# Kernel optimization log

Measured on AMD Instinct MI355X. Metric: run time of the kernel, lower is better.

Reference implementation:

```python
import jax, jax.numpy as jnp
import numpy as np

D_MODEL, N_HEADS, D_HEAD = 1024, 16, 64
B, T = 4, 2048


def setup_inputs() -> dict:
    key = jax.random.key(0)
    k1, k2, k3 = jax.random.split(key, 3)
    x = jax.random.normal(k1, (B, T, D_MODEL), dtype=jnp.float32)
    w_qkv = jax.random.normal(k2, (3 * N_HEADS * D_HEAD, D_MODEL), dtype=jnp.float32) * 0.02
    w_out = jax.random.normal(k3, (D_MODEL, N_HEADS * D_HEAD), dtype=jnp.float32) * 0.02
    return {"x": x, "w_qkv": w_qkv, "w_out": w_out}


def reference(x, w_qkv, w_out):
    Bx, Tx, Dx = x.shape
    scale = D_HEAD ** (-0.5)
    qkv = jnp.einsum('btd,ed->bte', x, w_qkv)  # [B,T,3*H*Dh]
    q, k, v = jnp.split(qkv, 3, axis=-1)
    def heads(t):  # [B,T,H*Dh] -> [B,H,T,Dh]
        return t.reshape(Bx, Tx, N_HEADS, D_HEAD).transpose(0, 2, 1, 3)
    q, k, v = heads(q), heads(k), heads(v)
    att = jnp.einsum('bhqd,bhkd->bhqk', q, k) * scale
    causal = jnp.tril(jnp.ones((Tx, Tx), dtype=bool))
    att = jnp.where(causal, att, -jnp.inf)
    att = jax.nn.softmax(att, axis=-1)
    y = jnp.einsum('bhqk,bhkd->bhqd', att, v)
    y = y.transpose(0, 2, 1, 3).reshape(Bx, Tx, N_HEADS * D_HEAD)
    return jnp.einsum('bte,de->btd', y, w_out)
```

## Files before the change

kernel.cpp:

```cpp
#include <hip/hip_runtime.h>
#include <hip/hip_bf16.h>

#define T_SEQ   2048
#define HEADS   16
#define DH      64
#define DMODEL  1024
#define EQKV    3072

typedef __attribute__((ext_vector_type(8)))  __bf16 bf16x8;
typedef __attribute__((ext_vector_type(4)))  float  f32x4;
typedef __attribute__((ext_vector_type(16))) float  f32x16;
typedef unsigned short ushort_t;
typedef unsigned int   uint_t;

__device__ __forceinline__ ushort_t f2bfu(float x) {
    union { float f; uint_t u; } c; c.f = x;
    uint_t u = c.u;
    uint_t r = (u + 0x7fffu + ((u >> 16) & 1u)) >> 16;
    return (ushort_t)r;
}

__device__ __forceinline__ uint_t cvtpk(float lo, float hi) {
    uint_t r;
    asm volatile("v_cvt_pk_bf16_f32 %0, %1, %2" : "=v"(r) : "v"(lo), "v"(hi));
    return r;
}

__device__ __forceinline__ void gload16(const ushort_t* g, ushort_t* l) {
    __builtin_amdgcn_global_load_lds(
        (const __attribute__((address_space(1))) void*)g,
        (__attribute__((address_space(3))) void*)l,
        16, 0, 0);
}

__global__ void cvt_f32_bf16(const float* __restrict__ in, ushort_t* __restrict__ out, int n4) {
    int i = blockIdx.x * blockDim.x + threadIdx.x;
    if (i >= n4) return;
    const float4 v = ((const float4*)in)[i];
    ushort_t r0 = f2bfu(v.x), r1 = f2bfu(v.y), r2 = f2bfu(v.z), r3 = f2bfu(v.w);
    uint_t lo = (uint_t)r0 | ((uint_t)r1 << 16);
    uint_t hi = (uint_t)r2 | ((uint_t)r3 << 16);
    ((uint2*)out)[i] = make_uint2(lo, hi);
}

#define BM 128
#define BN 128
#define BK 32

template<bool OUT_BF16>
__global__ __launch_bounds__(256) void gemm_bt(const ushort_t* __restrict__ A,
                                               const ushort_t* __restrict__ Bt,
                                               void* __restrict__ Cv,
                                               int M, int N, int K) {
    __shared__ __align__(16) ushort_t As[BM * BK];
    __shared__ __align__(16) ushort_t Bs[BN * BK];

    const int tid  = threadIdx.x;
    const int bn   = blockIdx.x, bm = blockIdx.y;
    const int row0 = bm * BM, col0 = bn * BN;
    const int wid  = tid >> 6, lane = tid & 63;
    const int wr   = wid >> 1, wc = wid & 1;
    const int lr   = lane & 15, lg = lane >> 4;

    const int lrow = lane >> 2;
    const int lcol = (lane & 3) * 8;

    f32x4 acc[4][4] = {};

    for (int k0 = 0; k0 < K; k0 += BK) {
        #pragma unroll
        for (int it = 0; it < 2; ++it) {
            const int c = wid * 2 + it;
            const int r = c * 16 + lrow;
            gload16(&A [(size_t)(row0 + r) * K + k0 + lcol], &As[c * 512]);
            gload16(&Bt[(size_t)(col0 + r) * K + k0 + lcol], &Bs[c * 512]);
        }
        __syncthreads();

        bf16x8 bfr[4];
        #pragma unroll
        for (int n = 0; n < 4; ++n)
            bfr[n] = *(const bf16x8*)&Bs[(wc * 64 + n * 16 + lr) * BK + lg * 8];
        #pragma unroll
        for (int m = 0; m < 4; ++m) {
            bf16x8 a = *(const bf16x8*)&As[(wr * 64 + m * 16 + lr) * BK + lg * 8];
            #pragma unroll
            for (int n = 0; n < 4; ++n)
                acc[m][n] = __builtin_amdgcn_mfma_f32_16x16x32_bf16(a, bfr[n], acc[m][n], 0, 0, 0);
        }
        __syncthreads();
    }

    #pragma unroll
    for (int m = 0; m < 4; ++m) {
        int rowb = row0 + wr * 64 + m * 16 + lg * 4;
        #pragma unroll
        for (int n = 0; n < 4; ++n) {
            int col = col0 + wc * 64 + n * 16 + lr;
            #pragma unroll
            for (int i = 0; i < 4; ++i) {
                if (OUT_BF16)
                    ((ushort_t*)Cv)[(size_t)(rowb + i) * N + col] = f2bfu(acc[m][n][i]);
                else
                    ((float*)Cv)[(size_t)(rowb + i) * N + col] = acc[m][n][i];
            }
        }
    }
}

__global__ __launch_bounds__(128, 2) void attn_fwd(const ushort_t* __restrict__ qkv,
                                                   ushort_t* __restrict__ y) {
    const int flat = blockIdx.x;
    const int xcd  = flat & 7;
    const int s    = flat >> 3;
    const int bh   = xcd * 8 + (s & 7);
    const int bx   = 31 - (s >> 3);
    const int b    = bh >> 4, h = bh & 15;
    const int tid  = threadIdx.x, lane = tid & 63;
    const int wid  = tid >> 6;
    const int i    = lane & 31;
    const int hh   = lane >> 5;
    const int bT   = b * T_SEQ;

    __shared__ __align__(16) ushort_t Ks[2][64][72];
    __shared__ __align__(16) ushort_t Vt[2][64][72];

    const int q0 = bx * 64 + wid * 32;
    const int qg = q0 + i;

    bf16x8 qf[4];
    {
        const ushort_t* qrow = qkv + (size_t)(bT + qg) * EQKV + h * DH;
        #pragma unroll
        for (int kd = 0; kd < 4; ++kd)
            qf[kd] = *(const bf16x8*)&qrow[kd * 16 + hh * 8];
    }

    float m = -1e30f, lsum = 0.f;
    f32x16 o0 = {}, o1 = {};

    const int nt = bx + 1;

    #pragma unroll
    for (int it = 0; it < 4; ++it) {
        const int idx = tid + it * 128;
        const int r   = idx >> 3;
        const int cc  = (idx & 7) * 8;
        const size_t go = (size_t)(bT + r) * EQKV + h * DH + cc;
        uint4 kk = *(const uint4*)&qkv[go + 1024];
        uint4 vv = *(const uint4*)&qkv[go + 2048];
        *(uint4*)&Ks[0][r][cc] = kk;
        const ushort_t* vs = (const ushort_t*)&vv;
        const int chunk = r >> 3, br = r & 7;
        #pragma unroll
        for (int j = 0; j < 8; ++j) {
            int dh = cc + j;
            Vt[0][dh][((chunk ^ (dh >> 3)) << 3) | br] = vs[j];
        }
    }
    __syncthreads();

    for (int t = 0; t < nt; ++t) {
        const int cb = t & 1, nb = cb ^ 1;
        const bool has_next = (t + 1 < nt);

        uint4 kr[4], vr[4];
        if (has_next) {
            #pragma unroll
            for (int it = 0; it < 4; ++it) {
                const int idx = tid + it * 128;
                const int r   = idx >> 3;
                const int cc  = (idx & 7) * 8;
                const size_t go = (size_t)(bT + (t + 1) * 64 + r) * EQKV + h * DH + cc;
                kr[it] = *(const uint4*)&qkv[go + 1024];
                vr[it] = *(const uint4*)&qkv[go + 2048];
            }
        }

        const int kmin = t * 64;
        const bool needmask = (kmin + 63) > q0;

        f32x16 st[2] = {};
        __builtin_amdgcn_s_setprio(1);
        #pragma unroll
        for (int kd = 0; kd < 4; ++kd) {
            bf16x8 ka0 = *(const bf16x8*)&Ks[cb][i][kd * 16 + hh * 8];
            bf16x8 ka1 = *(const bf16x8*)&Ks[cb][32 + i][kd * 16 + hh * 8];
            st[0] = __builtin_amdgcn_mfma_f32_32x32x16_bf16(ka0, qf[kd], st[0], 0, 0, 0);
            st[1] = __builtin_amdgcn_mfma_f32_32x32x16_bf16(ka1, qf[kd], st[1], 0, 0, 0);
        }
        __builtin_amdgcn_s_setprio(0);

        float pm = -1e30f;
        #pragma unroll
        for (int g = 0; g < 2; ++g) {
            #pragma unroll
            for (int r = 0; r < 16; ++r) {
                float v = st[g][r];
                if (needmask) {
                    int kv = kmin + g * 32 + (r & 3) + 8 * (r >> 2) + 4 * hh;
                    v = (kv <= qg) ? v : -1e30f;
                    st[g][r] = v;
                }
                pm = fmaxf(pm, v);
            }
        }
        pm = fmaxf(pm, __shfl_xor(pm, 32));

        if (!__all(pm - m <= 64.f)) {
            const float mnew = fmaxf(m, pm);
            const float corr = __expf((m - mnew) * 0.125f);
            m = mnew;
            lsum *= corr;
            #pragma unroll
            for (int r = 0; r < 16; ++r) { o0[r] *= corr; o1[r] *= corr; }
        }
        float rs = 0.f;
        #pragma unroll
        for (int g = 0; g < 2; ++g) {
            #pragma unroll
            for (int r = 0; r < 16; ++r) {
                float p = __expf((st[g][r] - m) * 0.125f);
                st[g][r] = p;
                rs += p;
            }
        }
        rs += __shfl_xor(rs, 32);
        lsum += rs;

        if (has_next) {
            #pragma unroll
            for (int it = 0; it < 4; ++it) {
                const int idx = tid + it * 128;
                const int r   = idx >> 3;
                const int cc  = (idx & 7) * 8;
                *(uint4*)&Ks[nb][r][cc] = kr[it];
                const ushort_t* vs = (const ushort_t*)&vr[it];
                const int chunk = r >> 3, br = r & 7;
                #pragma unroll
                for (int j = 0; j < 8; ++j) {
                    int dh = cc + j;
                    Vt[nb][dh][((chunk ^ (dh >> 3)) << 3) | br] = vs[j];
                }
            }
        }

        #pragma unroll
        for (int ks = 0; ks < 4; ++ks) {
            const int g = ks >> 1, b0 = (ks & 1) * 8;
            uint_t w0 = cvtpk(st[g][b0 + 0], st[g][b0 + 1]);
            uint_t w1 = cvtpk(st[g][b0 + 2], st[g][b0 + 3]);
            uint_t w2 = cvtpk(st[g][b0 + 4], st[g][b0 + 5]);
            uint_t w3 = cvtpk(st[g][b0 + 6], st[g][b0 + 7]);
            uint_t e0 = (uint_t)__shfl_xor((int)w0, 32);
            uint_t e1 = (uint_t)__shfl_xor((int)w1, 32);
            uint_t e2 = (uint_t)__shfl_xor((int)w2, 32);
            uint_t e3 = (uint_t)__shfl_xor((int)w3, 32);
            union { uint_t u[4]; bf16x8 v; } fr;
            fr.u[0] = hh ? e2 : w0;
            fr.u[1] = hh ? e3 : w1;
            fr.u[2] = hh ? w2 : e0;
            fr.u[3] = hh ? w3 : e1;
            const int cp0 = (((2 * ks + hh) ^ (i >> 3)) << 3);
            const int cp1 = (((2 * ks + hh) ^ (4 + (i >> 3))) << 3);
            bf16x8 va0 = *(const bf16x8*)&Vt[cb][i][cp0];
            bf16x8 va1 = *(const bf16x8*)&Vt[cb][32 + i][cp1];
            __builtin_amdgcn_s_setprio(1);
            o0 = __builtin_amdgcn_mfma_f32_32x32x16_bf16(va0, fr.v, o0, 0, 0, 0);
            o1 = __builtin_amdgcn_mfma_f32_32x32x16_bf16(va1, fr.v, o1, 0, 0, 0);
            __builtin_amdgcn_s_setprio(0);
        }

        __syncthreads();
    }

    const float inv = 1.f / lsum;
    ushort_t* yrow = y + (size_t)(bT + qg) * (HEADS * DH) + h * DH;
    #pragma unroll
    for (int df = 0; df < 2; ++df) {
        const f32x16 oo = df ? o1 : o0;
        #pragma unroll
        for (int q4 = 0; q4 < 4; ++q4) {
            uint_t w0 = cvtpk(oo[q4 * 4 + 0] * inv, oo[q4 * 4 + 1] * inv);
            uint_t w1 = cvtpk(oo[q4 * 4 + 2] * inv, oo[q4 * 4 + 3] * inv);
            uint2 pk = make_uint2(w0, w1);
            *(uint2*)&yrow[df * 32 + q4 * 8 + hh * 4] = pk;
        }
    }
}

extern "C" void kernel_launch(void* const* d_in, const int* in_sizes, int n_in,
                              void* d_out, int out_size, void* d_ws, size_t ws_size,
                              hipStream_t stream) {
    const float* x     = (const float*)d_in[0];
    const float* w_qkv = (const float*)d_in[1];
    const float* w_out = (const float*)d_in[2];

    const int BT = 4 * T_SEQ;

    char* ws = (char*)d_ws;
    ushort_t* xb   = (ushort_t*)(ws);
    ushort_t* wqb  = (ushort_t*)(ws + 16777216);
    ushort_t* wob  = (ushort_t*)(ws + 16777216 + 6291456);
    ushort_t* qkvb = (ushort_t*)(ws + 16777216 + 6291456 + 2097152);
    ushort_t* yb   = (ushort_t*)(ws + 16777216 + 6291456 + 2097152 + 50331648);

    {
        int n4 = (BT * DMODEL) / 4;
        cvt_f32_bf16<<<(n4 + 255) / 256, 256, 0, stream>>>(x, xb, n4);
        n4 = (EQKV * DMODEL) / 4;
        cvt_f32_bf16<<<(n4 + 255) / 256, 256, 0, stream>>>(w_qkv, wqb, n4);
        n4 = (DMODEL * DMODEL) / 4;
        cvt_f32_bf16<<<(n4 + 255) / 256, 256, 0, stream>>>(w_out, wob, n4);
    }

    {
        dim3 grid(EQKV / BN, BT / BM);
        gemm_bt<true><<<grid, 256, 0, stream>>>(xb, wqb, (void*)qkvb, BT, EQKV, DMODEL);
    }

    {
        attn_fwd<<<2048, 128, 0, stream>>>(qkvb, yb);
    }

    {
        dim3 grid(DMODEL / BN, BT / BM);
        gemm_bt<false><<<grid, 256, 0, stream>>>(yb, wob, d_out, BT, DMODEL, DMODEL);
    }
}
```

Before: 306.8 us.

## Load K fragments directly from global, fold scale into Q, remap GEMM tiles

The attention kernel drops the K shared-memory staging and has each lane load its K MFMA fragments straight from global memory each tile. The softmax scale is folded into Q at load time, which removes the per-element multiply in the exp path and tightens the lazy-rescale threshold to match. Occupancy is raised to 3 workgroups per CU now that LDS use is halved. The GEMM also gets an XCD-aware block-index remap for L2 locality. The risks are extra global and L2 traffic from uncoalesced per-lane K loads, exposed load latency because K is no longer prefetched, and an extra bf16 rounding of the scaled Q.

Result: slower. 365.3 us (+19.1%).

```diff
diff --git a/kernel.cpp b/kernel.cpp
--- a/kernel.cpp
+++ b/kernel.cpp
@@ -56,7 +56,11 @@
     __shared__ __align__(16) ushort_t Bs[BN * BK];
 
     const int tid  = threadIdx.x;
-    const int bn   = blockIdx.x, bm = blockIdx.y;
+    const int gx   = gridDim.x;
+    int flat = blockIdx.y * gx + blockIdx.x;
+    const int nwg  = gx * gridDim.y;
+    flat = (flat & 7) * (nwg >> 3) + (flat >> 3);
+    const int bn   = flat % gx, bm = flat / gx;
     const int row0 = bm * BM, col0 = bn * BN;
     const int wid  = tid >> 6, lane = tid & 63;
     const int wr   = wid >> 1, wc = wid & 1;
@@ -108,7 +112,7 @@
     }
 }
 
-__global__ __launch_bounds__(128, 2) void attn_fwd(const ushort_t* __restrict__ qkv,
+__global__ __launch_bounds__(128, 3) void attn_fwd(const ushort_t* __restrict__ qkv,
                                                    ushort_t* __restrict__ y) {
     const int flat = blockIdx.x;
     const int xcd  = flat & 7;
@@ -122,7 +126,6 @@
     const int hh   = lane >> 5;
     const int bT   = b * T_SEQ;
 
-    __shared__ __align__(16) ushort_t Ks[2][64][72];
     __shared__ __align__(16) ushort_t Vt[2][64][72];
 
     const int q0 = bx * 64 + wid * 32;
@@ -132,8 +135,14 @@
     {
         const ushort_t* qrow = qkv + (size_t)(bT + qg) * EQKV + h * DH;
         #pragma unroll
-        for (int kd = 0; kd < 4; ++kd)
-            qf[kd] = *(const bf16x8*)&qrow[kd * 16 + hh * 8];
+        for (int kd = 0; kd < 4; ++kd) {
+            bf16x8 q = *(const bf16x8*)&qrow[kd * 16 + hh * 8];
+            #pragma unroll
+            for (int j = 0; j < 8; ++j)
+                ((ushort_t*)&q)[j] = f2bfu(__bfloat162float(
+                    *(const __hip_bfloat16*)&((ushort_t*)&q)[j]) * 0.125f);
+            qf[kd] = q;
+        }
     }
 
     float m = -1e30f, lsum = 0.f;
@@ -147,9 +156,7 @@
         const int r   = idx >> 3;
         const int cc  = (idx & 7) * 8;
         const size_t go = (size_t)(bT + r) * EQKV + h * DH + cc;
-        uint4 kk = *(const uint4*)&qkv[go + 1024];
         uint4 vv = *(const uint4*)&qkv[go + 2048];
-        *(uint4*)&Ks[0][r][cc] = kk;
         const ushort_t* vs = (const ushort_t*)&vv;
         const int chunk = r >> 3, br = r & 7;
         #pragma unroll
@@ -163,8 +170,21 @@
     for (int t = 0; t < nt; ++t) {
         const int cb = t & 1, nb = cb ^ 1;
         const bool has_next = (t + 1 < nt);
-
-        uint4 kr[4], vr[4];
+        const int kmin = t * 64;
+
+        bf16x8 ka0[4], ka1[4];
+        {
+            const ushort_t* kbase = qkv + (size_t)(bT + kmin) * EQKV + 1024 + h * DH;
+            const ushort_t* k0p = kbase + (size_t)i * EQKV + hh * 8;
+            const ushort_t* k1p = kbase + (size_t)(32 + i) * EQKV + hh * 8;
+            #pragma unroll
+            for (int kd = 0; kd < 4; ++kd) {
+                ka0[kd] = *(const bf16x8*)&k0p[kd * 16];
+                ka1[kd] = *(const bf16x8*)&k1p[kd * 16];
+            }
+        }
+
+        uint4 vr[4];
         if (has_next) {
             #pragma unroll
             for (int it = 0; it < 4; ++it) {
@@ -172,22 +192,18 @@
                 const int r   = idx >> 3;
                 const int cc  = (idx & 7) * 8;
                 const size_t go = (size_t)(bT + (t + 1) * 64 + r) * EQKV + h * DH + cc;
-                kr[it] = *(const uint4*)&qkv[go + 1024];
                 vr[it] = *(const uint4*)&qkv[go + 2048];
             }
         }
 
-        const int kmin = t * 64;
         const bool needmask = (kmin + 63) > q0;
 
         f32x16 st[2] = {};
         __builtin_amdgcn_s_setprio(1);
         #pragma unroll
         for (int kd = 0; kd < 4; ++kd) {
-            bf16x8 ka0 = *(const bf16x8*)&Ks[cb][i][kd * 16 + hh * 8];
-            bf16x8 ka1 = *(const bf16x8*)&Ks[cb][32 + i][kd * 16 + hh * 8];
-            st[0] = __builtin_amdgcn_mfma_f32_32x32x16_bf16(ka0, qf[kd], st[0], 0, 0, 0);
-            st[1] = __builtin_amdgcn_mfma_f32_32x32x16_bf16(ka1, qf[kd], st[1], 0, 0, 0);
+            st[0] = __builtin_amdgcn_mfma_f32_32x32x16_bf16(ka0[kd], qf[kd], st[0], 0, 0, 0);
+            st[1] = __builtin_amdgcn_mfma_f32_32x32x16_bf16(ka1[kd], qf[kd], st[1], 0, 0, 0);
         }
         __builtin_amdgcn_s_setprio(0);
 
@@ -207,9 +223,9 @@
         }
         pm = fmaxf(pm, __shfl_xor(pm, 32));
 
-        if (!__all(pm - m <= 64.f)) {
+        if (!__all(pm - m <= 8.f)) {
             const float mnew = fmaxf(m, pm);
-            const float corr = __expf((m - mnew) * 0.125f);
+            const float corr = __expf(m - mnew);
             m = mnew;
             lsum *= corr;
             #pragma unroll
@@ -220,7 +236,7 @@
         for (int g = 0; g < 2; ++g) {
             #pragma unroll
             for (int r = 0; r < 16; ++r) {
-                float p = __expf((st[g][r] - m) * 0.125f);
+                float p = __expf(st[g][r] - m);
                 st[g][r] = p;
                 rs += p;
             }
@@ -234,7 +250,6 @@
                 const int idx = tid + it * 128;
                 const int r   = idx >> 3;
                 const int cc  = (idx & 7) * 8;
-                *(uint4*)&Ks[nb][r][cc] = kr[it];
                 const ushort_t* vs = (const ushort_t*)&vr[it];
                 const int chunk = r >> 3, br = r & 7;
                 #pragma unroll
```
